# Performance work log

Hardware: AMD Instinct MI355X
Metric: run time of the kernel (lower is better)

## Reference

```python
import jax, jax.numpy as jnp
import numpy as np

N_NODES = 100000
N_EDGES = 3200000


def gcn_conv(x, edge_index, W, b, n_nodes):
    # PyG GCNConv: x' = D^{-1/2} (A + I) D^{-1/2} (x W) + b
    h = x @ W  # [N, C_out]
    loop = jnp.arange(n_nodes, dtype=edge_index.dtype)
    src = jnp.concatenate([edge_index[0], loop])  # source nodes j
    dst = jnp.concatenate([edge_index[1], loop])  # target nodes i (aggregation)
    deg = jax.ops.segment_sum(jnp.ones_like(dst, h.dtype), dst, num_segments=n_nodes)
    dinv = jnp.where(deg > 0, jax.lax.rsqrt(deg), 0.0)
    norm = dinv[src] * dinv[dst]  # [E+N]
    msg = h[src] * norm[:, None]  # gather + scale
    out = jax.ops.segment_sum(msg, dst, num_segments=n_nodes)  # scatter-add
    return out + b


def setup_inputs() -> dict:
    key = jax.random.key(0)
    ks = jax.random.split(key, 6)
    x = jax.random.normal(ks[0], (N_NODES, 1), dtype=jnp.float32)
    edge_index = jax.random.randint(ks[1], (2, N_EDGES), 0, N_NODES, dtype=jnp.int64)
    W1 = jax.random.normal(ks[2], (1, 16), dtype=jnp.float32) * (1.0 / np.sqrt(1))
    b1 = jnp.zeros((16,), dtype=jnp.float32)
    W2 = jax.random.normal(ks[3], (16, 16), dtype=jnp.float32) * (1.0 / np.sqrt(16))
    b2 = jnp.zeros((16,), dtype=jnp.float32)
    Wl = jax.random.normal(ks[4], (16, 1), dtype=jnp.float32) * (1.0 / np.sqrt(16))
    bl = jnp.zeros((1,), dtype=jnp.float32)
    return {"x": x, "edge_index": edge_index, "W1": W1, "b1": b1,
            "W2": W2, "b2": b2, "Wl": Wl, "bl": bl}


def reference(x, edge_index, W1, b1, W2, b2, Wl, bl):
    n = x.shape[0]
    h = gcn_conv(x, edge_index, W1, b1, n)
    h = jax.nn.relu(h)
    # F.dropout(training=self.training): identity in eval mode
    h = gcn_conv(h, edge_index, W2, b2, n)
    return h @ Wl + bl  # [N, 1]
```

## Files before the change

### kernel.cpp

```cpp
#include <hip/hip_runtime.h>

#define N_NODES  100000
#define N_EDGES  3200000
#define NB       8
#define BN       12544
#define NBLK     256
#define THR      1024
#define QPB      (N_EDGES / NBLK / 4)
#define CAP      2048
#define SA       32
#define SPS      (NBLK / SA)
#define GA       (NB * SA)
#define REDB     ((N_NODES + THR - 1) / THR)


__global__ __launch_bounds__(THR) void k_route(
        const int* __restrict__ ei, unsigned* __restrict__ cnt,
        unsigned* __restrict__ pedge) {
    __shared__ __align__(16) unsigned stag[BN];
    __shared__ unsigned bcnt[NB], bbase[NB], bcur[NB];
    const int tid = threadIdx.x, blk = blockIdx.x;
    if (tid < NB) bcnt[tid] = 0u;
    __syncthreads();

    const uint4* s4 = (const uint4*)ei;
    const uint4* d4 = (const uint4*)(ei + N_EDGES);
    const int q0 = blk * QPB;
    uint4 dq[4], sq[4];
    #pragma unroll
    for (int i = 0; i < 4; ++i) {
        const int q = tid + i * THR;
        if (q < QPB) { dq[i] = d4[q0 + q]; sq[i] = s4[q0 + q]; }
    }

    unsigned c01 = 0, c23 = 0;
    #pragma unroll
    for (int i = 0; i < 4; ++i) {
        const int q = tid + i * THR;
        if (q < QPB) {
            const unsigned dd[4] = { dq[i].x, dq[i].y, dq[i].z, dq[i].w };
            #pragma unroll
            for (int k = 0; k < 4; ++k) {
                const unsigned b = dd[k] / BN;
                if (b < 4) c01 += 1u << (8 * b);
                else       c23 += 1u << (8 * (b - 4));
            }
        }
    }
    #pragma unroll
    for (int b = 0; b < 4; ++b) {
        const unsigned v0 = (c01 >> (8 * b)) & 0xFFu;
        const unsigned v1 = (c23 >> (8 * b)) & 0xFFu;
        if (v0) atomicAdd(&bcnt[b], v0);
        if (v1) atomicAdd(&bcnt[b + 4], v1);
    }
    __syncthreads();
    if (tid == 0) {
        unsigned run = 0;
        #pragma unroll
        for (int b = 0; b < NB; ++b) { bbase[b] = run; bcur[b] = run; run += bcnt[b]; }
    }
    __syncthreads();

    #pragma unroll
    for (int i = 0; i < 4; ++i) {
        const int q = tid + i * THR;
        if (q < QPB) {
            const unsigned dd[4] = { dq[i].x, dq[i].y, dq[i].z, dq[i].w };
            const unsigned ss[4] = { sq[i].x, sq[i].y, sq[i].z, sq[i].w };
            #pragma unroll
            for (int k = 0; k < 4; ++k) {
                const unsigned d = dd[k];
                const unsigned b = d / BN;
                const unsigned slot = atomicAdd(&bcur[b], 1u);
                stag[slot] = ss[k] | ((d - b * BN) << 17);
            }
        }
    }
    __syncthreads();

    #pragma unroll
    for (int b = 0; b < NB; ++b) {
        const unsigned n = bcnt[b] < CAP ? bcnt[b] : CAP;
        const unsigned base = bbase[b];
        unsigned* reg = pedge + ((size_t)(blk * NB + b)) * CAP;
        for (unsigned j = tid; j < n; j += THR) reg[j] = stag[base + j];
    }
    if (tid < NB) cnt[blk * NB + tid] = bcnt[tid] < CAP ? bcnt[tid] : CAP;
}

__global__ __launch_bounds__(THR) void k_acc(
        const unsigned* __restrict__ pedge, const unsigned* __restrict__ cnt,
        const float* __restrict__ vals, float* __restrict__ partials,
        const int degmode) {
    __shared__ __align__(16) float facc[BN];
    const int tid = threadIdx.x;
    const int bu = blockIdx.x / SA, sub = blockIdx.x % SA;
    for (int i = tid; i < BN; i += THR) facc[i] = 0.f;
    __syncthreads();
    for (int s = 0; s < SPS; ++s) {
        const int r = (sub * SPS + s) * NB + bu;
        const unsigned n = cnt[r];
        const unsigned* reg = pedge + (size_t)r * CAP;
        if (degmode) {
            for (unsigned j = tid; j < n; j += THR)
                atomicAdd(&facc[reg[j] >> 17], 1.f);
        } else {
            for (unsigned j = tid; j < n; j += THR) {
                const unsigned w = reg[j];
                atomicAdd(&facc[w >> 17], vals[w & 0x1FFFFu]);
            }
        }
    }
    __syncthreads();
    float4* po = (float4*)(partials + (size_t)blockIdx.x * BN);
    const float4* fi = (const float4*)facc;
    for (int i = tid; i < BN / 4; i += THR) po[i] = fi[i];
}

__device__ __forceinline__ float sum_partials(const float* __restrict__ partials,
                                              int g) {
    const int bu = g / BN, l = g - bu * BN;
    const float* pp = partials + (size_t)(bu * SA) * BN + l;
    float s = 0.f;
    #pragma unroll
    for (int k = 0; k < SA; ++k) s += pp[(size_t)k * BN];
    return s;
}

__global__ __launch_bounds__(THR) void k_red1(const float* __restrict__ x,
        const float* __restrict__ partials,
        float* __restrict__ dinv, float* __restrict__ xs) {
    const int g = blockIdx.x * THR + threadIdx.x;
    if (g >= N_NODES) return;
    const float deg = sum_partials(partials, g);
    const float di = rsqrtf(deg + 1.f);
    dinv[g] = di;
    xs[g] = x[g] * di;
}

__global__ __launch_bounds__(THR) void k_red2(const float* __restrict__ x,
        const float* __restrict__ partials, const float* __restrict__ dinv,
        const float* __restrict__ W1, const float* __restrict__ b1,
        const float* __restrict__ W2, const float* __restrict__ Wl,
        float* __restrict__ us, float* __restrict__ uself) {
    const int g = blockIdx.x * THR + threadIdx.x;
    if (g >= N_NODES) return;
    const float sum = sum_partials(partials, g);
    const float di = dinv[g];
    const float s1 = di * sum + x[g] * di * di;
    float u = 0.f;
    #pragma unroll
    for (int c = 0; c < 16; ++c) {
        float vcc = 0.f;
        #pragma unroll
        for (int k = 0; k < 16; ++k) vcc += W2[c * 16 + k] * Wl[k];
        u += fmaxf(W1[c] * s1 + b1[c], 0.f) * vcc;
    }
    us[g] = u * di;
    uself[g] = u * di * di;
}

__global__ __launch_bounds__(THR) void k_red3(const float* __restrict__ partials,
        const float* __restrict__ dinv, const float* __restrict__ uself,
        const float* __restrict__ W2, const float* __restrict__ b2,
        const float* __restrict__ Wl, const float* __restrict__ bl,
        float* __restrict__ out) {
    const int g = blockIdx.x * THR + threadIdx.x;
    if (g >= N_NODES) return;
    const float sum = sum_partials(partials, g);
    float vcb = bl[0];
    #pragma unroll
    for (int c = 0; c < 16; ++c) {
        float vcc = 0.f;
        #pragma unroll
        for (int k = 0; k < 16; ++k) vcc += W2[c * 16 + k] * Wl[k];
        vcb += b2[c] * vcc;
    }
    out[g] = dinv[g] * sum + uself[g] + vcb;
}

extern "C" void kernel_launch(void* const* d_in, const int* in_sizes, int n_in,
                              void* d_out, int out_size, void* d_ws, size_t ws_size,
                              hipStream_t stream) {
    const float* x  = (const float*)d_in[0];
    const int*   ei = (const int*)d_in[1];
    const float* W1 = (const float*)d_in[2];
    const float* b1 = (const float*)d_in[3];
    const float* W2 = (const float*)d_in[4];
    const float* b2 = (const float*)d_in[5];
    const float* Wl = (const float*)d_in[6];
    const float* bl = (const float*)d_in[7];
    float* out = (float*)d_out;

    unsigned* cnt      = (unsigned*)d_ws;
    unsigned* pedge    = cnt + NBLK * NB;
    float*    partials = (float*)(pedge + (size_t)NBLK * NB * CAP);
    float*    dinv     = partials + (size_t)GA * BN;
    float*    xs       = dinv + N_NODES;
    float*    us       = xs + N_NODES;
    float*    uself    = us + N_NODES;

    k_route<<<NBLK, THR, 0, stream>>>(ei, cnt, pedge);
    k_acc  <<<GA,   THR, 0, stream>>>(pedge, cnt, (const float*)0, partials, 1);
    k_red1 <<<REDB, THR, 0, stream>>>(x, partials, dinv, xs);
    k_acc  <<<GA,   THR, 0, stream>>>(pedge, cnt, xs, partials, 0);
    k_red2 <<<REDB, THR, 0, stream>>>(x, partials, dinv, W1, b1, W2, Wl, us, uself);
    k_acc  <<<GA,   THR, 0, stream>>>(pedge, cnt, us, partials, 0);
    k_red3 <<<REDB, THR, 0, stream>>>(partials, dinv, uself, W2, b2, Wl, bl, out);
}
```

Baseline: 197.4 us.

## Fuse degree counting into routing kernel with packed 16-bit counters

Degree counting moves out of a separate accumulation pass and into extra blocks of the routing kernel. Those blocks scan destination slices and keep packed 16-bit counts in shared memory, which removes one k_acc launch and its large float partials write and read. The reduction kernels now use 256-thread blocks, red1 handles two nodes per thread, and k_acc reads packed edges as uint4 and issues four gathers before its atomics. The cost is that 64 extra blocks each read a slice of all destinations, and the 16-bit counters could overflow for very high degrees.

```diff
diff --git a/kernel.cpp b/kernel.cpp
--- a/kernel.cpp
+++ b/kernel.cpp
@@ -4,27 +4,59 @@
 #define N_EDGES  3200000
 #define NB       8
 #define BN       12544
-#define NBLK     256
+#define BNH      (BN / 2)
+#define NRT      256
+#define NDG      64
+#define DSL      8
 #define THR      1024
-#define QPB      (N_EDGES / NBLK / 4)
+#define QPB      (N_EDGES / NRT / 4)
+#define QDS      (N_EDGES / DSL / 4)
 #define CAP      2048
 #define SA       32
-#define SPS      (NBLK / SA)
+#define SPS      (NRT / SA)
 #define GA       (NB * SA)
-#define REDB     ((N_NODES + THR - 1) / THR)
-
-
-__global__ __launch_bounds__(THR) void k_route(
+#define TRD      256
+
+
+__global__ __launch_bounds__(THR) void k_route_deg(
         const int* __restrict__ ei, unsigned* __restrict__ cnt,
-        unsigned* __restrict__ pedge) {
-    __shared__ __align__(16) unsigned stag[BN];
+        unsigned* __restrict__ pedge, unsigned* __restrict__ pdeg) {
+    __shared__ __align__(16) unsigned smem[BN];
     __shared__ unsigned bcnt[NB], bbase[NB], bcur[NB];
-    const int tid = threadIdx.x, blk = blockIdx.x;
+    const int tid = threadIdx.x;
+    const uint4* d4 = (const uint4*)(ei + N_EDGES);
+
+    if (blockIdx.x < NDG) {
+        const int bu = blockIdx.x >> 3, s = blockIdx.x & 7;
+        for (int i = tid; i < BNH; i += THR) smem[i] = 0u;
+        __syncthreads();
+        const unsigned base_node = (unsigned)bu * BN;
+        const int q1 = (s + 1) * QDS;
+        #pragma unroll 2
+        for (int q = s * QDS + tid; q < q1; q += THR) {
+            const uint4 dv = d4[q];
+            const unsigned dd[4] = { dv.x, dv.y, dv.z, dv.w };
+            #pragma unroll
+            for (int k = 0; k < 4; ++k) {
+                const unsigned d = dd[k];
+                if (d / BN == (unsigned)bu) {
+                    const unsigned dl = d - base_node;
+                    atomicAdd(&smem[dl >> 1], 1u << ((dl & 1) << 4));
+                }
+            }
+        }
+        __syncthreads();
+        uint4* po = (uint4*)(pdeg + (size_t)blockIdx.x * BNH);
+        const uint4* fi = (const uint4*)smem;
+        for (int i = tid; i < BNH / 4; i += THR) po[i] = fi[i];
+        return;
+    }
+
+    const int blk = blockIdx.x - NDG;
     if (tid < NB) bcnt[tid] = 0u;
     __syncthreads();
 
     const uint4* s4 = (const uint4*)ei;
-    const uint4* d4 = (const uint4*)(ei + N_EDGES);
     const int q0 = blk * QPB;
     uint4 dq[4], sq[4];
     #pragma unroll
@@ -73,7 +105,7 @@
                 const unsigned d = dd[k];
                 const unsigned b = d / BN;
                 const unsigned slot = atomicAdd(&bcur[b], 1u);
-                stag[slot] = ss[k] | ((d - b * BN) << 17);
+                smem[slot] = ss[k] | ((d - b * BN) << 17);
             }
         }
     }
@@ -84,32 +116,40 @@
         const unsigned n = bcnt[b] < CAP ? bcnt[b] : CAP;
         const unsigned base = bbase[b];
         unsigned* reg = pedge + ((size_t)(blk * NB + b)) * CAP;
-        for (unsigned j = tid; j < n; j += THR) reg[j] = stag[base + j];
+        for (unsigned j = tid; j < n; j += THR) reg[j] = smem[base + j];
     }
     if (tid < NB) cnt[blk * NB + tid] = bcnt[tid] < CAP ? bcnt[tid] : CAP;
 }
 
 __global__ __launch_bounds__(THR) void k_acc(
         const unsigned* __restrict__ pedge, const unsigned* __restrict__ cnt,
-        const float* __restrict__ vals, float* __restrict__ partials,
-        const int degmode) {
+        const float* __restrict__ vals, float* __restrict__ partials) {
     __shared__ __align__(16) float facc[BN];
     const int tid = threadIdx.x;
     const int bu = blockIdx.x / SA, sub = blockIdx.x % SA;
-    for (int i = tid; i < BN; i += THR) facc[i] = 0.f;
+    for (int i = tid; i < BN / 4; i += THR)
+        ((float4*)facc)[i] = make_float4(0.f, 0.f, 0.f, 0.f);
     __syncthreads();
     for (int s = 0; s < SPS; ++s) {
         const int r = (sub * SPS + s) * NB + bu;
         const unsigned n = cnt[r];
         const unsigned* reg = pedge + (size_t)r * CAP;
-        if (degmode) {
-            for (unsigned j = tid; j < n; j += THR)
-                atomicAdd(&facc[reg[j] >> 17], 1.f);
-        } else {
-            for (unsigned j = tid; j < n; j += THR) {
-                const unsigned w = reg[j];
-                atomicAdd(&facc[w >> 17], vals[w & 0x1FFFFu]);
-            }
+        const uint4* reg4 = (const uint4*)reg;
+        const unsigned n4 = n >> 2;
+        for (unsigned j = tid; j < n4; j += THR) {
+            const uint4 w = reg4[j];
+            const float v0 = vals[w.x & 0x1FFFFu];
+            const float v1 = vals[w.y & 0x1FFFFu];
+            const float v2 = vals[w.z & 0x1FFFFu];
+            const float v3 = vals[w.w & 0x1FFFFu];
+            atomicAdd(&facc[w.x >> 17], v0);
+            atomicAdd(&facc[w.y >> 17], v1);
+            atomicAdd(&facc[w.z >> 17], v2);
+            atomicAdd(&facc[w.w >> 17], v3);
+        }
+        for (unsigned j = (n4 << 2) + tid; j < n; j += THR) {
+            const unsigned w = reg[j];
+            atomicAdd(&facc[w >> 17], vals[w & 0x1FFFFu]);
         }
     }
     __syncthreads();
@@ -128,23 +168,33 @@
     return s;
 }
 
-__global__ __launch_bounds__(THR) void k_red1(const float* __restrict__ x,
-        const float* __restrict__ partials,
+__global__ __launch_bounds__(TRD) void k_red1(const float* __restrict__ x,
+        const unsigned* __restrict__ pdeg,
         float* __restrict__ dinv, float* __restrict__ xs) {
-    const int g = blockIdx.x * THR + threadIdx.x;
-    if (g >= N_NODES) return;
-    const float deg = sum_partials(partials, g);
-    const float di = rsqrtf(deg + 1.f);
-    dinv[g] = di;
-    xs[g] = x[g] * di;
-}
-
-__global__ __launch_bounds__(THR) void k_red2(const float* __restrict__ x,
+    const int t = blockIdx.x * TRD + threadIdx.x;
+    const int g0 = 2 * t;
+    if (g0 >= N_NODES) return;
+    const int bu = g0 / BN, l = g0 - bu * BN;
+    const unsigned* pp = pdeg + (size_t)(bu * DSL) * BNH + (l >> 1);
+    unsigned r0 = 0, r1 = 0;
+    #pragma unroll
+    for (int s = 0; s < DSL; ++s) {
+        const unsigned w = pp[(size_t)s * BNH];
+        r0 += w & 0xFFFFu; r1 += w >> 16;
+    }
+    const float di0 = rsqrtf((float)r0 + 1.f);
+    const float di1 = rsqrtf((float)r1 + 1.f);
+    const float2 xv = *(const float2*)(x + g0);
+    *(float2*)(dinv + g0) = make_float2(di0, di1);
+    *(float2*)(xs + g0)   = make_float2(xv.x * di0, xv.y * di1);
+}
+
+__global__ __launch_bounds__(TRD) void k_red2(const float* __restrict__ x,
         const float* __restrict__ partials, const float* __restrict__ dinv,
         const float* __restrict__ W1, const float* __restrict__ b1,
         const float* __restrict__ W2, const float* __restrict__ Wl,
         float* __restrict__ us, float* __restrict__ uself) {
-    const int g = blockIdx.x * THR + threadIdx.x;
+    const int g = blockIdx.x * TRD + threadIdx.x;
     if (g >= N_NODES) return;
     const float sum = sum_partials(partials, g);
     const float di = dinv[g];
@@ -161,12 +211,12 @@
     uself[g] = u * di * di;
 }
 
-__global__ __launch_bounds__(THR) void k_red3(const float* __restrict__ partials,
+__global__ __launch_bounds__(TRD) void k_red3(const float* __restrict__ partials,
         const float* __restrict__ dinv, const float* __restrict__ uself,
         const float* __restrict__ W2, const float* __restrict__ b2,
         const float* __restrict__ Wl, const float* __restrict__ bl,
         float* __restrict__ out) {
-    const int g = blockIdx.x * THR + threadIdx.x;
+    const int g = blockIdx.x * TRD + threadIdx.x;
     if (g >= N_NODES) return;
     const float sum = sum_partials(partials, g);
     float vcb = bl[0];
@@ -194,18 +244,21 @@
     float* out = (float*)d_out;
 
     unsigned* cnt      = (unsigned*)d_ws;
-    unsigned* pedge    = cnt + NBLK * NB;
-    float*    partials = (float*)(pedge + (size_t)NBLK * NB * CAP);
-    float*    dinv     = partials + (size_t)GA * BN;
+    unsigned* pedge    = cnt + NRT * NB;
+    float*    partials = (float*)(pedge + (size_t)NRT * NB * CAP);
+    unsigned* pdeg     = (unsigned*)(partials + (size_t)GA * BN);
+    float*    dinv     = (float*)(pdeg + (size_t)NDG * BNH);
     float*    xs       = dinv + N_NODES;
     float*    us       = xs + N_NODES;
     float*    uself    = us + N_NODES;
 
-    k_route<<<NBLK, THR, 0, stream>>>(ei, cnt, pedge);
-    k_acc  <<<GA,   THR, 0, stream>>>(pedge, cnt, (const float*)0, partials, 1);
-    k_red1 <<<REDB, THR, 0, stream>>>(x, partials, dinv, xs);
-    k_acc  <<<GA,   THR, 0, stream>>>(pedge, cnt, xs, partials, 0);
-    k_red2 <<<REDB, THR, 0, stream>>>(x, partials, dinv, W1, b1, W2, Wl, us, uself);
-    k_acc  <<<GA,   THR, 0, stream>>>(pedge, cnt, us, partials, 0);
-    k_red3 <<<REDB, THR, 0, stream>>>(partials, dinv, uself, W2, b2, Wl, bl, out);
-}
+    const int rb1 = (N_NODES / 2 + TRD - 1) / TRD;
+    const int rb  = (N_NODES + TRD - 1) / TRD;
+
+    k_route_deg<<<NDG + NRT, THR, 0, stream>>>(ei, cnt, pedge, pdeg);
+    k_red1 <<<rb1, TRD, 0, stream>>>(x, pdeg, dinv, xs);
+    k_acc  <<<GA,  THR, 0, stream>>>(pedge, cnt, xs, partials);
+    k_red2 <<<rb,  TRD, 0, stream>>>(x, partials, dinv, W1, b1, W2, Wl, us, uself);
+    k_acc  <<<GA,  THR, 0, stream>>>(pedge, cnt, us, partials);
+    k_red3 <<<rb,  TRD, 0, stream>>>(partials, dinv, uself, W2, b2, Wl, bl, out);
+}
```

New measurement: 189.6 us. -4.0%, faster.
